# Optimization experiments

Measured on AMD Instinct MI355X. Metric: run time of the kernel, lower is better.

## Reference

```python
import jax, jax.numpy as jnp
import numpy as np

CE_WEIGHT = 1.0
TRIPLET_WEIGHT = 0.1
MARGIN = 0.2


def setup_inputs() -> dict:
    key = jax.random.key(0)
    k1, k2, k3 = jax.random.split(key, 3)
    B, D, V = 4096, 512, 6000
    logits = jax.random.normal(k1, (B, V), dtype=jnp.float32)
    embeddings = jax.random.normal(k2, (B, D), dtype=jnp.float32)
    labels = jax.random.randint(k3, (B,), 0, 512, dtype=jnp.int64)
    return {"logits": logits, "embeddings": embeddings, "labels": labels}


def _pairwise_dist(emb):
    # Euclidean cdist via gram matrix; safe sqrt (zero grad where d2 == 0).
    sq = jnp.sum(emb * emb, axis=-1)  # [B]
    d2 = sq[:, None] + sq[None, :] - 2.0 * (emb @ emb.T)  # [B, B]
    d2 = jnp.maximum(d2, 0.0)
    safe = jnp.where(d2 > 0.0, d2, 1.0)
    return jnp.where(d2 > 0.0, jnp.sqrt(safe), 0.0)


def _losses(logits, embeddings, labels):
    B = logits.shape[0]
    # Cross entropy (mean reduction, matching nn.CrossEntropyLoss).
    logp = jax.nn.log_softmax(logits, axis=-1)
    ce_loss = -jnp.mean(jnp.take_along_axis(logp, labels[:, None], axis=1)[:, 0])

    # Batch-hard triplet loss, fully vectorized (one masked amax/amin per row).
    dist = _pairwise_dist(embeddings)  # [B, B]
    same = labels[:, None] == labels[None, :]  # [B, B]
    eye = jnp.eye(B, dtype=bool)
    pos_mask = same & ~eye
    neg_mask = ~same
    neg_inf = jnp.float32(-np.inf)
    pos_inf = jnp.float32(np.inf)
    hardest_pos = jnp.max(jnp.where(pos_mask, dist, neg_inf), axis=1)  # [B]
    hardest_neg = jnp.min(jnp.where(neg_mask, dist, pos_inf), axis=1)  # [B]
    valid = jnp.any(pos_mask, axis=1) & jnp.any(neg_mask, axis=1)  # [B]
    per_row = jax.nn.relu(hardest_pos - hardest_neg + MARGIN)
    per_row = jnp.where(valid, per_row, 0.0)
    n_valid = jnp.sum(valid.astype(jnp.float32))
    triplet_loss = jnp.where(n_valid > 0, jnp.sum(per_row) / jnp.maximum(n_valid, 1.0), 0.0)

    total_loss = CE_WEIGHT * ce_loss + TRIPLET_WEIGHT * triplet_loss
    return total_loss, ce_loss, triplet_loss


def reference(logits, embeddings, labels):
    return _losses(logits, embeddings, labels)
```

## Files before the change

kernel.cpp:

```cpp
#include <hip/hip_runtime.h>
#include <hip/hip_bf16.h>
#include <math.h>

#define BN   4096
#define DN   512
#define VN   6000
#define NCLS 512

typedef __attribute__((ext_vector_type(8)))  short short8;
typedef __attribute__((ext_vector_type(16))) float f32x16;

__device__ __forceinline__ unsigned short f2bf(float x) {
  unsigned int u = __float_as_uint(x);
  u = (u + 0x7FFFu + ((u >> 16) & 1u)) >> 16;
  return (unsigned short)u;
}

__device__ __forceinline__ void gld_lds16(const unsigned short* g, unsigned short* l) {
  __builtin_amdgcn_global_load_lds(
      (const __attribute__((address_space(1))) void*)g,
      (__attribute__((address_space(3))) void*)l, 16, 0, 0);
}

__launch_bounds__(128)
__global__ void prep_kernel(const float* __restrict__ emb, const int* __restrict__ labels,
                            unsigned short* __restrict__ embh, float* __restrict__ sqn,
                            int* __restrict__ cnt, int* __restrict__ posb,
                            int* __restrict__ negb) {
  int row = blockIdx.x;
  int tid = threadIdx.x;
  const float4* rp = (const float4*)(emb + (size_t)row * DN);
  float4 v = rp[tid];
  float ss = v.x * v.x + v.y * v.y + v.z * v.z + v.w * v.w;
  ushort4 h;
  h.x = f2bf(v.x); h.y = f2bf(v.y); h.z = f2bf(v.z); h.w = f2bf(v.w);
  ((ushort4*)(embh + (size_t)row * DN))[tid] = h;
#pragma unroll
  for (int off = 1; off < 64; off <<= 1) ss += __shfl_xor(ss, off);
  __shared__ float parts[2];
  if ((tid & 63) == 0) parts[tid >> 6] = ss;
  __syncthreads();
  if (tid == 0) {
    sqn[row] = parts[0] + parts[1];
    posb[row] = 0;
    negb[row] = 0x7F800000;
    atomicAdd(cnt + labels[row], 1);
  }
}

__launch_bounds__(256)
__global__ void ce_kernel(const float* __restrict__ logits,
                          const int* __restrict__ labels,
                          float* __restrict__ ce_part) {
  const int row = blockIdx.x;
  const float* rp = logits + (size_t)row * VN;
  const int tid = threadIdx.x;
  const int lab = labels[row];
  const float xlab = rp[lab];
  const float4* rp4 = (const float4*)rp;
  float4 v[6];
#pragma unroll
  for (int u = 0; u < 6; ++u) {
    int j = tid + u * 256;
    if (j < VN / 4) v[u] = rp4[j];
  }
  float s = 0.f;
#pragma unroll
  for (int u = 0; u < 6; ++u) {
    int j = tid + u * 256;
    if (j < VN / 4)
      s += __expf(v[u].x) + __expf(v[u].y) + __expf(v[u].z) + __expf(v[u].w);
  }
#pragma unroll
  for (int off = 1; off < 64; off <<= 1) s += __shfl_xor(s, off);
  __shared__ float sp[4];
  if ((tid & 63) == 0) sp[tid >> 6] = s;
  __syncthreads();
  if (tid == 0) {
    float S = sp[0] + sp[1] + sp[2] + sp[3];
    ce_part[row] = logf(S) - xlab;
  }
}

__launch_bounds__(256)
__global__ void triplet_kernel(const unsigned short* __restrict__ embh,
                               const float* __restrict__ sqn,
                               const int* __restrict__ labels,
                               int* __restrict__ posb, int* __restrict__ negb) {
  __shared__ unsigned short sA[128 * 64];
  __shared__ unsigned short sB[128 * 64];

  const int tid  = threadIdx.x;
  const int lane = tid & 63;
  const int w    = tid >> 6;
  const int m    = lane & 31;
  const int half = lane >> 5;
  const int i0   = blockIdx.y * 128;
  const int j0   = blockIdx.x * 128;

  const unsigned short* src = (w < 2) ? (embh + (size_t)i0 * DN)
                                      : (embh + (size_t)j0 * DN);
  unsigned short* dst = (w < 2) ? sA : sB;
  const int rbase = (w & 1) * 64;
  const int lrow  = lane >> 3;
  const int lchk  = (lane & 7) ^ lrow;
  const unsigned short* g0 = src + (size_t)(rbase + lrow) * DN + lchk * 8;

  const int qi = (w & 1) * 64;
  const int qj = (w >> 1) * 64;

  f32x16 acc[2][2] = {};

  for (int ks = 0; ks < 8; ++ks) {
    const int kk = ks * 64;
    __syncthreads();
#pragma unroll
    for (int s = 0; s < 8; ++s) {
      gld_lds16(g0 + kk + (size_t)s * 8 * DN, dst + (rbase + s * 8) * 64);
    }
    __syncthreads();

#pragma unroll
    for (int t = 0; t < 4; ++t) {
      const int c = t * 2 + half;
      const int ra0 = qi + m, ra1 = qi + 32 + m;
      const int rb0 = qj + m, rb1 = qj + 32 + m;
      short8 a0 = *(const short8*)(sA + ra0 * 64 + ((c ^ (ra0 & 7)) * 8));
      short8 a1 = *(const short8*)(sA + ra1 * 64 + ((c ^ (ra1 & 7)) * 8));
      short8 b0 = *(const short8*)(sB + rb0 * 64 + ((c ^ (rb0 & 7)) * 8));
      short8 b1 = *(const short8*)(sB + rb1 * 64 + ((c ^ (rb1 & 7)) * 8));
      acc[0][0] = __builtin_amdgcn_mfma_f32_32x32x16_bf16(a0, b0, acc[0][0], 0, 0, 0);
      acc[0][1] = __builtin_amdgcn_mfma_f32_32x32x16_bf16(a0, b1, acc[0][1], 0, 0, 0);
      acc[1][0] = __builtin_amdgcn_mfma_f32_32x32x16_bf16(a1, b0, acc[1][0], 0, 0, 0);
      acc[1][1] = __builtin_amdgcn_mfma_f32_32x32x16_bf16(a1, b1, acc[1][1], 0, 0, 0);
    }
  }

  const int gj0 = j0 + qj + m;
  const int gj1 = gj0 + 32;
  const int cl0 = labels[gj0], cl1 = labels[gj1];
  const float cq0 = sqn[gj0], cq1 = sqn[gj1];
  float pj0 = 0.f, pj1 = 0.f, nj0 = INFINITY, nj1 = INFINITY;

#pragma unroll
  for (int rb = 0; rb < 2; ++rb) {
#pragma unroll
    for (int r = 0; r < 16; ++r) {
      const int gi = i0 + qi + rb * 32 + (r & 3) + 8 * (r >> 2) + 4 * half;
      const int rl = labels[gi];
      const float rq = sqn[gi];
      const float d20 = fmaf(-2.f, acc[rb][0][r], rq + cq0);
      const float d21 = fmaf(-2.f, acc[rb][1][r], rq + cq1);
      if (rl == cl0) { if (gi != gj0) pj0 = fmaxf(pj0, d20); }
      else nj0 = fminf(nj0, d20);
      if (rl == cl1) { if (gi != gj1) pj1 = fmaxf(pj1, d21); }
      else nj1 = fminf(nj1, d21);
    }
  }
  pj0 = fmaxf(pj0, __shfl_xor(pj0, 32));
  nj0 = fminf(nj0, __shfl_xor(nj0, 32));
  pj1 = fmaxf(pj1, __shfl_xor(pj1, 32));
  nj1 = fminf(nj1, __shfl_xor(nj1, 32));
  if (half == 0) {
    atomicMax(posb + gj0, __float_as_int(pj0));
    atomicMin(negb + gj0, __float_as_int(nj0));
    atomicMax(posb + gj1, __float_as_int(pj1));
    atomicMin(negb + gj1, __float_as_int(nj1));
  }
}

__launch_bounds__(1024)
__global__ void finalize_kernel(const int* __restrict__ posb, const int* __restrict__ negb,
                                const int* __restrict__ labels, const int* __restrict__ cnt,
                                const float* __restrict__ ce_part, float* __restrict__ out) {
  const int tid = threadIdx.x;
  float cesum = 0.f, sum = 0.f, nv = 0.f;
#pragma unroll
  for (int u = 0; u < 4; ++u) {
    const int i = tid + u * 1024;
    cesum += ce_part[i];
    int c = cnt[labels[i]];
    float p = sqrtf(fmaxf(__int_as_float(posb[i]), 0.f));
    float n = sqrtf(fmaxf(__int_as_float(negb[i]), 0.f));
    float t = fmaxf(p - n + 0.2f, 0.f);
    if (c >= 2 && c < BN) { sum += t; nv += 1.f; }
  }
#pragma unroll
  for (int off = 1; off < 64; off <<= 1) {
    cesum += __shfl_xor(cesum, off);
    sum   += __shfl_xor(sum, off);
    nv    += __shfl_xor(nv, off);
  }
  __shared__ float s0[16], s1[16], s2[16];
  if ((tid & 63) == 0) { s0[tid >> 6] = cesum; s1[tid >> 6] = sum; s2[tid >> 6] = nv; }
  __syncthreads();
  if (tid == 0) {
    cesum = 0.f; sum = 0.f; nv = 0.f;
#pragma unroll
    for (int wv = 0; wv < 16; ++wv) { cesum += s0[wv]; sum += s1[wv]; nv += s2[wv]; }
    float trip = (nv > 0.f) ? sum / nv : 0.f;
    float ce = cesum * (1.f / BN);
    out[0] = ce + 0.1f * trip;
    out[1] = ce;
    out[2] = trip;
  }
}

extern "C" void kernel_launch(void* const* d_in, const int* in_sizes, int n_in,
                              void* d_out, int out_size, void* d_ws, size_t ws_size,
                              hipStream_t stream) {
  const float* logits = (const float*)d_in[0];
  const float* emb    = (const float*)d_in[1];
  const int*   labels = (const int*)d_in[2];
  float* out = (float*)d_out;

  char* ws = (char*)d_ws;
  unsigned short* embh = (unsigned short*)ws;
  float* sqn    = (float*)(ws + (size_t)BN * DN * 2);
  int*   posb   = (int*)((char*)sqn  + (size_t)BN * 4);
  int*   negb   = (int*)((char*)posb + (size_t)BN * 4);
  int*   cnt    = (int*)((char*)negb + (size_t)BN * 4);
  float* ce_part = (float*)((char*)cnt + (size_t)NCLS * 4);

  hipMemsetAsync(cnt, 0, (size_t)NCLS * 4, stream);
  hipLaunchKernelGGL(prep_kernel, dim3(BN), dim3(128), 0, stream,
                     emb, labels, embh, sqn, cnt, posb, negb);
  hipLaunchKernelGGL(ce_kernel, dim3(BN), dim3(256), 0, stream,
                     logits, labels, ce_part);
  hipLaunchKernelGGL(triplet_kernel, dim3(32, 32), dim3(256), 0, stream,
                     embh, sqn, labels, posb, negb);
  hipLaunchKernelGGL(finalize_kernel, dim3(1), dim3(1024), 0, stream,
                     posb, negb, labels, cnt, ce_part, out);
}
```

Before: 193.3 us.

## Exploit distance symmetry with triangular tiling of single-wave triplet blocks

Launches only the upper-triangular 64x64 tiles of the pairwise distance matrix and computes both A·Bᵀ and B·Aᵀ in the same block. Each tile then updates the hardest positive and negative for both its row and column sets. Blocks shrink to one wave with a 64-row tile and raw waitcnt in place of barriers. This cuts redundant global loads of tile pairs, but each block now does twice the MFMAs with less reuse and no load/compute overlap.

```diff
diff --git a/kernel.cpp b/kernel.cpp
--- a/kernel.cpp
+++ b/kernel.cpp
@@ -82,90 +82,117 @@
   }
 }
 
-__launch_bounds__(256)
+__launch_bounds__(64, 2)
 __global__ void triplet_kernel(const unsigned short* __restrict__ embh,
                                const float* __restrict__ sqn,
                                const int* __restrict__ labels,
                                int* __restrict__ posb, int* __restrict__ negb) {
-  __shared__ unsigned short sA[128 * 64];
-  __shared__ unsigned short sB[128 * 64];
-
-  const int tid  = threadIdx.x;
-  const int lane = tid & 63;
-  const int w    = tid >> 6;
-  const int m    = lane & 31;
+  __shared__ unsigned short sA[64 * 64];
+  __shared__ unsigned short sB[64 * 64];
+
+  const int lane = threadIdx.x;
+  const int m = lane & 31;
   const int half = lane >> 5;
-  const int i0   = blockIdx.y * 128;
-  const int j0   = blockIdx.x * 128;
-
-  const unsigned short* src = (w < 2) ? (embh + (size_t)i0 * DN)
-                                      : (embh + (size_t)j0 * DN);
-  unsigned short* dst = (w < 2) ? sA : sB;
-  const int rbase = (w & 1) * 64;
-  const int lrow  = lane >> 3;
-  const int lchk  = (lane & 7) ^ lrow;
-  const unsigned short* g0 = src + (size_t)(rbase + lrow) * DN + lchk * 8;
-
-  const int qi = (w & 1) * 64;
-  const int qj = (w >> 1) * 64;
+
+  const int t = blockIdx.x;
+  int J = (int)((sqrtf(8.f * (float)t + 1.f) - 1.f) * 0.5f);
+  while ((J + 1) * (J + 2) / 2 <= t) ++J;
+  while (J * (J + 1) / 2 > t) --J;
+  const int I = t - J * (J + 1) / 2;
+  const int i0 = I * 64, j0 = J * 64;
+  const bool diag = (I == J);
+
+  const int lrow = lane >> 3;
+  const int lchk = (lane & 7) ^ lrow;
+  const unsigned short* gA = embh + (size_t)(i0 + lrow) * DN + lchk * 8;
+  const unsigned short* gB = embh + (size_t)(j0 + lrow) * DN + lchk * 8;
 
   f32x16 acc[2][2] = {};
+  f32x16 accT[2][2] = {};
 
   for (int ks = 0; ks < 8; ++ks) {
     const int kk = ks * 64;
-    __syncthreads();
-#pragma unroll
-    for (int s = 0; s < 8; ++s) {
-      gld_lds16(g0 + kk + (size_t)s * 8 * DN, dst + (rbase + s * 8) * 64);
-    }
-    __syncthreads();
-
-#pragma unroll
-    for (int t = 0; t < 4; ++t) {
-      const int c = t * 2 + half;
-      const int ra0 = qi + m, ra1 = qi + 32 + m;
-      const int rb0 = qj + m, rb1 = qj + 32 + m;
-      short8 a0 = *(const short8*)(sA + ra0 * 64 + ((c ^ (ra0 & 7)) * 8));
-      short8 a1 = *(const short8*)(sA + ra1 * 64 + ((c ^ (ra1 & 7)) * 8));
-      short8 b0 = *(const short8*)(sB + rb0 * 64 + ((c ^ (rb0 & 7)) * 8));
-      short8 b1 = *(const short8*)(sB + rb1 * 64 + ((c ^ (rb1 & 7)) * 8));
-      acc[0][0] = __builtin_amdgcn_mfma_f32_32x32x16_bf16(a0, b0, acc[0][0], 0, 0, 0);
-      acc[0][1] = __builtin_amdgcn_mfma_f32_32x32x16_bf16(a0, b1, acc[0][1], 0, 0, 0);
-      acc[1][0] = __builtin_amdgcn_mfma_f32_32x32x16_bf16(a1, b0, acc[1][0], 0, 0, 0);
-      acc[1][1] = __builtin_amdgcn_mfma_f32_32x32x16_bf16(a1, b1, acc[1][1], 0, 0, 0);
-    }
-  }
-
-  const int gj0 = j0 + qj + m;
-  const int gj1 = gj0 + 32;
-  const int cl0 = labels[gj0], cl1 = labels[gj1];
-  const float cq0 = sqn[gj0], cq1 = sqn[gj1];
-  float pj0 = 0.f, pj1 = 0.f, nj0 = INFINITY, nj1 = INFINITY;
-
-#pragma unroll
-  for (int rb = 0; rb < 2; ++rb) {
-#pragma unroll
-    for (int r = 0; r < 16; ++r) {
-      const int gi = i0 + qi + rb * 32 + (r & 3) + 8 * (r >> 2) + 4 * half;
-      const int rl = labels[gi];
-      const float rq = sqn[gi];
-      const float d20 = fmaf(-2.f, acc[rb][0][r], rq + cq0);
-      const float d21 = fmaf(-2.f, acc[rb][1][r], rq + cq1);
-      if (rl == cl0) { if (gi != gj0) pj0 = fmaxf(pj0, d20); }
-      else nj0 = fminf(nj0, d20);
-      if (rl == cl1) { if (gi != gj1) pj1 = fmaxf(pj1, d21); }
-      else nj1 = fminf(nj1, d21);
-    }
-  }
-  pj0 = fmaxf(pj0, __shfl_xor(pj0, 32));
-  nj0 = fminf(nj0, __shfl_xor(nj0, 32));
-  pj1 = fmaxf(pj1, __shfl_xor(pj1, 32));
-  nj1 = fminf(nj1, __shfl_xor(nj1, 32));
-  if (half == 0) {
-    atomicMax(posb + gj0, __float_as_int(pj0));
-    atomicMin(negb + gj0, __float_as_int(nj0));
-    atomicMax(posb + gj1, __float_as_int(pj1));
-    atomicMin(negb + gj1, __float_as_int(nj1));
+    asm volatile("s_waitcnt lgkmcnt(0)" ::: "memory");
+#pragma unroll
+    for (int s = 0; s < 8; ++s)
+      gld_lds16(gA + kk + (size_t)s * 8 * DN, &sA[s * 8 * 64]);
+#pragma unroll
+    for (int s = 0; s < 8; ++s)
+      gld_lds16(gB + kk + (size_t)s * 8 * DN, &sB[s * 8 * 64]);
+    asm volatile("s_waitcnt vmcnt(0)" ::: "memory");
+#pragma unroll
+    for (int q = 0; q < 4; ++q) {
+      const int c = q * 2 + half;
+      const int sw = ((c ^ (m & 7)) * 8);
+      short8 a0 = *(const short8*)&sA[m * 64 + sw];
+      short8 a1 = *(const short8*)&sA[(32 + m) * 64 + sw];
+      short8 b0 = *(const short8*)&sB[m * 64 + sw];
+      short8 b1 = *(const short8*)&sB[(32 + m) * 64 + sw];
+      acc[0][0]  = __builtin_amdgcn_mfma_f32_32x32x16_bf16(a0, b0, acc[0][0], 0, 0, 0);
+      acc[0][1]  = __builtin_amdgcn_mfma_f32_32x32x16_bf16(a0, b1, acc[0][1], 0, 0, 0);
+      acc[1][0]  = __builtin_amdgcn_mfma_f32_32x32x16_bf16(a1, b0, acc[1][0], 0, 0, 0);
+      acc[1][1]  = __builtin_amdgcn_mfma_f32_32x32x16_bf16(a1, b1, acc[1][1], 0, 0, 0);
+      accT[0][0] = __builtin_amdgcn_mfma_f32_32x32x16_bf16(b0, a0, accT[0][0], 0, 0, 0);
+      accT[0][1] = __builtin_amdgcn_mfma_f32_32x32x16_bf16(b0, a1, accT[0][1], 0, 0, 0);
+      accT[1][0] = __builtin_amdgcn_mfma_f32_32x32x16_bf16(b1, a0, accT[1][0], 0, 0, 0);
+      accT[1][1] = __builtin_amdgcn_mfma_f32_32x32x16_bf16(b1, a1, accT[1][1], 0, 0, 0);
+    }
+  }
+
+  {
+    const int gj0 = j0 + m, gj1 = j0 + 32 + m;
+    const int cl0 = labels[gj0], cl1 = labels[gj1];
+    const float cq0 = sqn[gj0], cq1 = sqn[gj1];
+    float p0 = 0.f, p1 = 0.f, n0 = INFINITY, n1 = INFINITY;
+#pragma unroll
+    for (int rb = 0; rb < 2; ++rb) {
+#pragma unroll
+      for (int r = 0; r < 16; ++r) {
+        const int gi = i0 + rb * 32 + (r & 3) + 8 * (r >> 2) + 4 * half;
+        const int rl = labels[gi];
+        const float rq = sqn[gi];
+        const float d0 = fmaf(-2.f, acc[rb][0][r], rq + cq0);
+        const float d1 = fmaf(-2.f, acc[rb][1][r], rq + cq1);
+        if (rl == cl0) { if (gi != gj0) p0 = fmaxf(p0, d0); } else n0 = fminf(n0, d0);
+        if (rl == cl1) { if (gi != gj1) p1 = fmaxf(p1, d1); } else n1 = fminf(n1, d1);
+      }
+    }
+    p0 = fmaxf(p0, __shfl_xor(p0, 32)); n0 = fminf(n0, __shfl_xor(n0, 32));
+    p1 = fmaxf(p1, __shfl_xor(p1, 32)); n1 = fminf(n1, __shfl_xor(n1, 32));
+    if (half == 0) {
+      atomicMax(posb + gj0, __float_as_int(p0));
+      atomicMin(negb + gj0, __float_as_int(n0));
+      atomicMax(posb + gj1, __float_as_int(p1));
+      atomicMin(negb + gj1, __float_as_int(n1));
+    }
+  }
+
+  if (!diag) {
+    const int gj0 = i0 + m, gj1 = i0 + 32 + m;
+    const int cl0 = labels[gj0], cl1 = labels[gj1];
+    const float cq0 = sqn[gj0], cq1 = sqn[gj1];
+    float p0 = 0.f, p1 = 0.f, n0 = INFINITY, n1 = INFINITY;
+#pragma unroll
+    for (int rb = 0; rb < 2; ++rb) {
+#pragma unroll
+      for (int r = 0; r < 16; ++r) {
+        const int gi = j0 + rb * 32 + (r & 3) + 8 * (r >> 2) + 4 * half;
+        const int rl = labels[gi];
+        const float rq = sqn[gi];
+        const float d0 = fmaf(-2.f, accT[rb][0][r], rq + cq0);
+        const float d1 = fmaf(-2.f, accT[rb][1][r], rq + cq1);
+        if (rl == cl0) p0 = fmaxf(p0, d0); else n0 = fminf(n0, d0);
+        if (rl == cl1) p1 = fmaxf(p1, d1); else n1 = fminf(n1, d1);
+      }
+    }
+    p0 = fmaxf(p0, __shfl_xor(p0, 32)); n0 = fminf(n0, __shfl_xor(n0, 32));
+    p1 = fmaxf(p1, __shfl_xor(p1, 32)); n1 = fminf(n1, __shfl_xor(n1, 32));
+    if (half == 0) {
+      atomicMax(posb + gj0, __float_as_int(p0));
+      atomicMin(negb + gj0, __float_as_int(n0));
+      atomicMax(posb + gj1, __float_as_int(p1));
+      atomicMin(negb + gj1, __float_as_int(n1));
+    }
   }
 }
 
@@ -227,7 +254,7 @@
                      emb, labels, embh, sqn, cnt, posb, negb);
   hipLaunchKernelGGL(ce_kernel, dim3(BN), dim3(256), 0, stream,
                      logits, labels, ce_part);
-  hipLaunchKernelGGL(triplet_kernel, dim3(32, 32), dim3(256), 0, stream,
+  hipLaunchKernelGGL(triplet_kernel, dim3(64 * 65 / 2), dim3(64), 0, stream,
                      embh, sqn, labels, posb, negb);
   hipLaunchKernelGGL(finalize_kernel, dim3(1), dim3(1024), 0, stream,
                      posb, negb, labels, cnt, ce_part, out);
```

New measurement: 191.9 us. Within noise of the previous version (-0.7%).
